# Kernel tuning notes

Measured on AMD Instinct MI355X. Metric: run time of the kernel, lower is better.

The kernel has to match this reference:

```python
import jax, jax.numpy as jnp
import numpy as np

N = 100000          # num nodes
E_C = 6_400_000     # connection edges
E_D = 400_000       # destination edges
F_IN = 5
H = 8
BN_EPS = 1e-5
L2_EPS = 1e-12


def setup_inputs() -> dict:
    key = jax.random.key(0)
    ks = jax.random.split(key, 16)
    d = {}
    d["x"] = jax.random.normal(ks[0], (N, F_IN), dtype=jnp.float32)
    d["edge_index_connections"] = jax.random.randint(ks[1], (2, E_C), 0, N, dtype=jnp.int64)
    d["edge_index_destinations"] = jax.random.randint(ks[2], (2, E_D), 0, N, dtype=jnp.int64)
    # SAGEConv weights: lin_l (neighbor aggregate), lin_r (root), no bias
    d["W1l"] = jax.random.normal(ks[3], (H, F_IN), jnp.float32) * 0.3
    d["W1r"] = jax.random.normal(ks[4], (H, F_IN), jnp.float32) * 0.3
    d["W2l"] = jax.random.normal(ks[5], (H, H), jnp.float32) * 0.3
    d["W2r"] = jax.random.normal(ks[6], (H, H), jnp.float32) * 0.3
    d["W3l"] = jax.random.normal(ks[7], (H, H), jnp.float32) * 0.3
    d["W3r"] = jax.random.normal(ks[8], (H, H), jnp.float32) * 0.3
    d["W4l"] = jax.random.normal(ks[9], (H, H), jnp.float32) * 0.3
    d["W4r"] = jax.random.normal(ks[10], (H, H), jnp.float32) * 0.3
    # LazyBatchNorm1d affine params (init gamma=1, beta=0)
    for i in range(1, 5):
        d[f"g{i}"] = jnp.ones((H,), jnp.float32)
        d[f"b{i}"] = jnp.zeros((H,), jnp.float32)
    return d


def _sage(x, ei, Wl, Wr):
    # PyG SAGEConv(mean aggr, normalize=True, bias=False):
    # out = lin_l(mean_{j in N(i)} x_j) + lin_r(x_i); then L2 normalize rows.
    src, dst = ei[0], ei[1]
    msgs = x[src]                                            # [E, F] gather
    s = jax.ops.segment_sum(msgs, dst, num_segments=N)       # [N, F]
    cnt = jax.ops.segment_sum(jnp.ones((ei.shape[1],), x.dtype), dst, num_segments=N)
    mean = s / jnp.maximum(cnt, 1.0)[:, None]                # zero for isolated nodes
    out = mean @ Wl.T + x @ Wr.T                             # [N, H]
    nrm = jnp.linalg.norm(out, axis=-1, keepdims=True)
    return out / jnp.maximum(nrm, L2_EPS)


def _bn(x, g, b):
    # BatchNorm1d in training mode: per-feature batch stats (biased variance)
    m = x.mean(axis=0)
    v = x.var(axis=0)
    return (x - m) * jax.lax.rsqrt(v + BN_EPS) * g + b


def reference(x, edge_index_connections, edge_index_destinations,
              W1l, W1r, W2l, W2r, W3l, W3r, W4l, W4r,
              g1, b1, g2, b2, g3, b3, g4, b4):
    eic = edge_index_connections
    eid = edge_index_destinations
    h = _bn(jax.nn.relu(_sage(x, eic, W1l, W1r)), g1, b1)
    # ITERATIONS_BEFORE_DESTINATION = 1 (conv4 + bn2)
    h = _bn(jax.nn.relu(_sage(h, eic, W4l, W4r)), g2, b2)
    # destination pass (conv2 + bn3)
    h = _bn(jax.nn.relu(_sage(h, eid, W2l, W2r)), g3, b3)
    # ITERATIONS_AFTER_DESTINATION = 2 (conv3 + bn4)
    for _ in range(2):
        h = _bn(jax.nn.relu(_sage(h, eic, W3l, W3r)), g4, b4)
    return h
```

## Files before the change

kernel.cpp:

```cpp
#include <hip/hip_runtime.h>
#include <hip/hip_fp16.h>

#define NN 100000
#define EC 6400000
#define ED 400000
#define BN_EPS 1e-5f
#define NSB ((NN + 255) >> 8)
#define NCH 256
#define CSR_CAP 19200
#define CHUNK_OF(E) (((((E) + NCH - 1) / NCH) + 3) & ~3)


__global__ __launch_bounds__(1024)
void pre_hist_prep(const int* __restrict__ eic, const int* __restrict__ eid,
                   int* __restrict__ bhist_c, int* __restrict__ bhist_d,
                   const float* __restrict__ x, const float* __restrict__ W1l,
                   const float* __restrict__ W1r, float* __restrict__ xp,
                   __half* __restrict__ xp16,
                   float* __restrict__ W1lp, float* __restrict__ W1rp) {
    int blk = blockIdx.x;
    if (blk < 2 * NCH) {
        const int* ei = (blk < NCH) ? eic : eid;
        int E = (blk < NCH) ? EC : ED;
        int* bhist = (blk < NCH) ? bhist_c : bhist_d;
        int k = (blk < NCH) ? blk : blk - NCH;
        __shared__ int h[NSB];
        for (int i = threadIdx.x; i < NSB; i += 1024) h[i] = 0;
        __syncthreads();
        int chunk = CHUNK_OF(E);
        int beg = k * chunk, end = min(E, beg + chunk);
        for (int e = beg + threadIdx.x * 4; e < end; e += 1024 * 4) {
            int4 d4 = *(const int4*)&ei[E + e];
            atomicAdd(&h[d4.x >> 8], 1);
            atomicAdd(&h[d4.y >> 8], 1);
            atomicAdd(&h[d4.z >> 8], 1);
            atomicAdd(&h[d4.w >> 8], 1);
        }
        __syncthreads();
        for (int i = threadIdx.x; i < NSB; i += 1024) bhist[i * NCH + k] = h[i];
    } else {
        int pb = blk - 2 * NCH;
        int t = pb * 1024 + threadIdx.x;
        if (t < 64) {
            int f = t >> 3, k = t & 7;
            W1lp[t] = (k < 5) ? W1l[f * 5 + k] : 0.f;
            W1rp[t] = (k < 5) ? W1r[f * 5 + k] : 0.f;
        }
        for (int idx = t; idx < NN * 8; idx += 32 * 1024) {
            int f = idx & 7, i = idx >> 3;
            float v = (f < 5) ? x[i * 5 + f] : 0.f;
            xp[idx] = v;
            xp16[idx] = __float2half(v);
        }
    }
}

__global__ __launch_bounds__(256)
void row_scan2(int* __restrict__ bhist_c, int* __restrict__ total_c,
               int* __restrict__ bhist_d, int* __restrict__ total_d) {
    int blk = blockIdx.x;
    int* row = (blk < NSB) ? (bhist_c + blk * NCH)
                           : (bhist_d + (blk - NSB) * NCH);
    int* total = (blk < NSB) ? total_c : total_d;
    int bb = (blk < NSB) ? blk : blk - NSB;
    __shared__ int wsum[4];
    int lane = threadIdx.x & 63, w = threadIdx.x >> 6;
    int v = row[threadIdx.x];
    int x = v;
    #pragma unroll
    for (int sh = 1; sh < 64; sh <<= 1) { int y = __shfl_up(x, sh); if (lane >= sh) x += y; }
    if (lane == 63) wsum[w] = x;
    __syncthreads();
    int wb = 0;
    #pragma unroll
    for (int j = 0; j < 4; ++j) if (j < w) wb += wsum[j];
    row[threadIdx.x] = wb + x - v;
    if (threadIdx.x == 255) total[bb] = wb + x;
}

__global__ void base2(const int* __restrict__ total_c, int* __restrict__ bbase_c,
                      const int* __restrict__ total_d, int* __restrict__ bbase_d,
                      float* __restrict__ stats) {
    for (int i = threadIdx.x; i < 5 * 256; i += 256) stats[i] = 0.f;
    __shared__ int wsum[4];
    __shared__ int carry;
    int lane = threadIdx.x & 63, w = threadIdx.x >> 6;
    for (int which = 0; which < 2; ++which) {
        const int* gt = which ? total_d : total_c;
        int* bb = which ? bbase_d : bbase_c;
        if (threadIdx.x == 0) carry = 0;
        __syncthreads();
        for (int s = 0; s < NSB; s += 256) {
            int idx = s + threadIdx.x;
            int v = (idx < NSB) ? gt[idx] : 0;
            int x = v;
            #pragma unroll
            for (int sh = 1; sh < 64; sh <<= 1) { int y = __shfl_up(x, sh); if (lane >= sh) x += y; }
            if (lane == 63) wsum[w] = x;
            __syncthreads();
            int wb = 0;
            #pragma unroll
            for (int j = 0; j < 4; ++j) if (j < w) wb += wsum[j];
            int all = wsum[0] + wsum[1] + wsum[2] + wsum[3];
            if (idx < NSB) bb[idx] = carry + wb + x - v;
            __syncthreads();
            if (threadIdx.x == 0) carry += all;
            __syncthreads();
        }
    }
}

__global__ __launch_bounds__(1024)
void scatter2(const int* __restrict__ eic, const int* __restrict__ eid,
              const int* __restrict__ bhist_c, const int* __restrict__ bbase_c,
              unsigned* __restrict__ packed_c,
              const int* __restrict__ bhist_d, const int* __restrict__ bbase_d,
              unsigned* __restrict__ packed_d) {
    int blk = blockIdx.x;
    const int* ei = (blk < NCH) ? eic : eid;
    int E = (blk < NCH) ? EC : ED;
    const int* bhist = (blk < NCH) ? bhist_c : bhist_d;
    const int* bbase = (blk < NCH) ? bbase_c : bbase_d;
    unsigned* packed = (blk < NCH) ? packed_c : packed_d;
    int k = (blk < NCH) ? blk : blk - NCH;
    __shared__ int cur[NSB];
    for (int b = threadIdx.x; b < NSB; b += 1024)
        cur[b] = bbase[b] + bhist[b * NCH + k];
    __syncthreads();
    int chunk = CHUNK_OF(E);
    int beg = k * chunk, end = min(E, beg + chunk);
    for (int e = beg + threadIdx.x * 4; e < end; e += 1024 * 4) {
        int4 s4 = *(const int4*)&ei[e];
        int4 d4 = *(const int4*)&ei[E + e];
        { int p = atomicAdd(&cur[d4.x >> 8], 1); packed[p] = (unsigned)s4.x | ((unsigned)(d4.x & 255) << 17); }
        { int p = atomicAdd(&cur[d4.y >> 8], 1); packed[p] = (unsigned)s4.y | ((unsigned)(d4.y & 255) << 17); }
        { int p = atomicAdd(&cur[d4.z >> 8], 1); packed[p] = (unsigned)s4.z | ((unsigned)(d4.z & 255) << 17); }
        { int p = atomicAdd(&cur[d4.w >> 8], 1); packed[p] = (unsigned)s4.w | ((unsigned)(d4.w & 255) << 17); }
    }
}

__global__ __launch_bounds__(256)
void csr2(const unsigned* __restrict__ packed_c, const int* __restrict__ bbase_c,
          const int* __restrict__ total_c, int* __restrict__ csr_c,
          int* __restrict__ offs_c, int* __restrict__ deg_c, float* __restrict__ inv_c,
          const unsigned* __restrict__ packed_d, const int* __restrict__ bbase_d,
          const int* __restrict__ total_d, int* __restrict__ csr_d,
          int* __restrict__ offs_d, int* __restrict__ deg_d, float* __restrict__ inv_d) {
    int blk = blockIdx.x;
    const unsigned* packed = (blk < NSB) ? packed_c : packed_d;
    const int* bbase = (blk < NSB) ? bbase_c : bbase_d;
    const int* total = (blk < NSB) ? total_c : total_d;
    int* csr  = (blk < NSB) ? csr_c : csr_d;
    int* offs = (blk < NSB) ? offs_c : offs_d;
    int* deg  = (blk < NSB) ? deg_c : deg_d;
    float* inv = (blk < NSB) ? inv_c : inv_d;
    int b = (blk < NSB) ? blk : blk - NSB;

    __shared__ int h[256];
    __shared__ int loff[256];
    __shared__ int ws2[4];
    __shared__ int ebuf[CSR_CAP];
    int ebeg = bbase[b], ecnt = total[b];
    int node0 = b << 8;
    int nn = min(256, NN - node0);
    h[threadIdx.x] = 0;
    __syncthreads();
    for (int e = threadIdx.x; e < ecnt; e += 256)
        atomicAdd(&h[packed[ebeg + e] >> 17], 1);
    __syncthreads();
    {
        int lane = threadIdx.x & 63, w = threadIdx.x >> 6;
        int v = h[threadIdx.x], x = v;
        #pragma unroll
        for (int sh = 1; sh < 64; sh <<= 1) { int y = __shfl_up(x, sh); if (lane >= sh) x += y; }
        if (lane == 63) ws2[w] = x;
        __syncthreads();
        int wb = 0;
        #pragma unroll
        for (int j = 0; j < 4; ++j) if (j < w) wb += ws2[j];
        int excl = wb + x - v;
        loff[threadIdx.x] = excl;
        if (threadIdx.x < nn) {
            int node = node0 + threadIdx.x;
            offs[node] = ebeg + excl;
            deg[node]  = v;
            inv[node]  = 1.0f / (float)(v > 1 ? v : 1);
        }
    }
    __syncthreads();
    if (ecnt <= CSR_CAP) {
        for (int e = threadIdx.x; e < ecnt; e += 256) {
            unsigned u = packed[ebeg + e];
            int p = atomicAdd(&loff[u >> 17], 1);
            ebuf[p] = (int)(u & 0x1FFFF);
        }
        __syncthreads();
        for (int e = threadIdx.x; e < ecnt; e += 256) csr[ebeg + e] = ebuf[e];
    } else {
        for (int e = threadIdx.x; e < ecnt; e += 256) {
            unsigned u = packed[ebeg + e];
            int p = atomicAdd(&loff[u >> 17], 1);
            csr[ebeg + p] = (int)(u & 0x1FFFF);
        }
    }
}

template<bool APPLY_BN>
__global__ __launch_bounds__(256)
void sage_layer8(const float* __restrict__ hin,
                 const __half* __restrict__ hin16,
                 const float* __restrict__ stats_in,
                 const float* __restrict__ gin, const float* __restrict__ bin,
                 const int* __restrict__ offs, const int* __restrict__ deg,
                 const int* __restrict__ csr, const float* __restrict__ inv,
                 const float* __restrict__ Wl, const float* __restrict__ Wr,
                 float* __restrict__ hout, __half* __restrict__ hout16,
                 float* __restrict__ stats_out) {
    __shared__ float bl[16];
    int tid = threadIdx.x;
    if (tid < 16) bl[tid] = 0.f;
    __syncthreads();
    int wave = tid >> 6, lane = tid & 63, g = lane >> 3, f = lane & 7;

    float sc[8], sh[8];
    #pragma unroll
    for (int k = 0; k < 8; ++k) { sc[k] = 1.f; sh[k] = 0.f; }
    if constexpr (APPLY_BN) {
        #pragma unroll
        for (int k = 0; k < 8; ++k) {
            float m = stats_in[k * 16] * (1.f / NN);
            float v = stats_in[(8 + k) * 16] * (1.f / NN) - m * m;
            float is = rsqrtf(v + BN_EPS);
            sc[k] = gin[k] * is;
            sh[k] = bin[k] - m * sc[k];
        }
    }
    float wl[8], wr[8];
    #pragma unroll
    for (int k = 0; k < 8; ++k) { wl[k] = Wl[f * 8 + k]; wr[k] = Wr[f * 8 + k]; }

    float acc_r = 0.f, acc_r2 = 0.f;
    const int stride = gridDim.x * 32;
    for (int i0 = (blockIdx.x * 4 + wave) * 8; i0 < NN; i0 += stride) {
        int i = i0 + g;
        int ic = min(i, NN - 1);
        bool ok = (i < NN);
        int d = ok ? deg[ic] : 0;
        int o = offs[ic];
        float a0 = 0, a1 = 0, a2 = 0, a3 = 0, a4 = 0, a5 = 0, a6 = 0, a7 = 0;
        for (int b = 0; b < d; b += 8) {
            int e = b + f;
            int cv = csr[o + e];
            float m = (e < d) ? 1.f : 0.f;
            unsigned s = min((unsigned)cv & 0x1FFFFu, (unsigned)(NN - 1));
            uint4 rv = *(const uint4*)(hin16 + (size_t)s * 8);
            float2 p0 = __half22float2(*(const __half2*)&rv.x);
            float2 p1 = __half22float2(*(const __half2*)&rv.y);
            float2 p2 = __half22float2(*(const __half2*)&rv.z);
            float2 p3 = __half22float2(*(const __half2*)&rv.w);
            a0 = fmaf(p0.x, m, a0); a1 = fmaf(p0.y, m, a1);
            a2 = fmaf(p1.x, m, a2); a3 = fmaf(p1.y, m, a3);
            a4 = fmaf(p2.x, m, a4); a5 = fmaf(p2.y, m, a5);
            a6 = fmaf(p3.x, m, a6); a7 = fmaf(p3.y, m, a7);
        }
        #pragma unroll
        for (int msk = 1; msk < 8; msk <<= 1) {
            a0 += __shfl_xor(a0, msk); a1 += __shfl_xor(a1, msk);
            a2 += __shfl_xor(a2, msk); a3 += __shfl_xor(a3, msk);
            a4 += __shfl_xor(a4, msk); a5 += __shfl_xor(a5, msk);
            a6 += __shfl_xor(a6, msk); a7 += __shfl_xor(a7, msk);
        }
        float im = inv[ic];
        float dnz = (d > 0) ? 1.f : 0.f;
        const float4* hp = (const float4*)(hin + (size_t)ic * 8);
        float4 h0 = hp[0];
        float4 h1 = hp[1];
        float hk[8] = { h0.x, h0.y, h0.z, h0.w, h1.x, h1.y, h1.z, h1.w };
        float ac[8] = { a0, a1, a2, a3, a4, a5, a6, a7 };
        float y = 0.f;
        #pragma unroll
        for (int k = 0; k < 8; ++k) {
            float mk = fmaf(sc[k], ac[k] * im, sh[k] * dnz);
            float hh = fmaf(sc[k], hk[k], sh[k]);
            y = fmaf(mk, wl[k], y);
            y = fmaf(hh, wr[k], y);
        }
        float n2 = y * y;
        n2 += __shfl_xor(n2, 1);
        n2 += __shfl_xor(n2, 2);
        n2 += __shfl_xor(n2, 4);
        float z = y / fmaxf(sqrtf(n2), 1e-12f);
        float r = fmaxf(z, 0.f);
        r = ok ? r : 0.f;
        if (ok) {
            hout[(size_t)i * 8 + f] = r;
            hout16[(size_t)i * 8 + f] = __float2half(r);
        }
        acc_r += r;
        acc_r2 += r * r;
    }
    atomicAdd(&bl[f], acc_r);
    atomicAdd(&bl[8 + f], acc_r2);
    __syncthreads();
    if (tid < 16) atomicAdd(&stats_out[tid * 16], bl[tid]);
}

__global__ void apply_bn_out(const float* __restrict__ hin,
                             const float* __restrict__ stats,
                             const float* __restrict__ g, const float* __restrict__ b,
                             float* __restrict__ out) {
    int t = blockIdx.x * blockDim.x + threadIdx.x;
    if (t >= NN * 8) return;
    int f = t & 7;
    float m = stats[f * 16] * (1.0f / NN);
    float v = stats[(8 + f) * 16] * (1.0f / NN) - m * m;
    float sc = g[f] * rsqrtf(v + BN_EPS);
    float sh = b[f] - m * sc;
    out[t] = fmaf(hin[t], sc, sh);
}


static inline char* bump(char*& p, size_t bytes) {
    char* r = p;
    p += (bytes + 255) & ~(size_t)255;
    return r;
}

extern "C" void kernel_launch(void* const* d_in, const int* in_sizes, int n_in,
                              void* d_out, int out_size, void* d_ws, size_t ws_size,
                              hipStream_t stream) {
    const float* x   = (const float*)d_in[0];
    const int* eic   = (const int*)d_in[1];
    const int* eid   = (const int*)d_in[2];
    const float* W1l = (const float*)d_in[3];
    const float* W1r = (const float*)d_in[4];
    const float* W2l = (const float*)d_in[5];
    const float* W2r = (const float*)d_in[6];
    const float* W3l = (const float*)d_in[7];
    const float* W3r = (const float*)d_in[8];
    const float* W4l = (const float*)d_in[9];
    const float* W4r = (const float*)d_in[10];
    const float* g1 = (const float*)d_in[11];
    const float* b1 = (const float*)d_in[12];
    const float* g2 = (const float*)d_in[13];
    const float* b2 = (const float*)d_in[14];
    const float* g3 = (const float*)d_in[15];
    const float* b3 = (const float*)d_in[16];
    const float* g4 = (const float*)d_in[17];
    const float* b4 = (const float*)d_in[18];
    float* out = (float*)d_out;

    char* p = (char*)d_ws;
    float* stats   = (float*)bump(p, 5 * 256 * 4);
    int*   bhist_c = (int*)  bump(p, (size_t)NSB * NCH * 4);
    int*   bhist_d = (int*)  bump(p, (size_t)NSB * NCH * 4);
    int*   total_c = (int*)  bump(p, NSB * 4);
    int*   bbase_c = (int*)  bump(p, NSB * 4);
    int*   total_d = (int*)  bump(p, NSB * 4);
    int*   bbase_d = (int*)  bump(p, NSB * 4);
    int*   offs_c  = (int*)  bump(p, NN * 4);
    int*   deg_c   = (int*)  bump(p, NN * 4);
    float* inv_c   = (float*)bump(p, NN * 4);
    int*   offs_d  = (int*)  bump(p, NN * 4);
    int*   deg_d   = (int*)  bump(p, NN * 4);
    float* inv_d   = (float*)bump(p, NN * 4);
    int*   csr_c   = (int*)  bump(p, ((size_t)EC + 64) * 4);
    int*   csr_d   = (int*)  bump(p, ((size_t)ED + 64) * 4);
    float* xp32    = (float*)bump(p, (size_t)NN * 8 * 4);
    __half* xp16   = (__half*)bump(p, (size_t)NN * 8 * 2);
    float* W1lp    = (float*)bump(p, 64 * 4);
    float* W1rp    = (float*)bump(p, 64 * 4);
    unsigned* packed_d = (unsigned*)bump(p, (size_t)ED * 4);
    char* pc = p;
    unsigned* packed_c = (unsigned*)bump(p, (size_t)EC * 4);
    char* pr = pc;
    float*  r_a   = (float*) bump(pr, (size_t)NN * 8 * 4);
    float*  r_b   = (float*) bump(pr, (size_t)NN * 8 * 4);
    __half* h16_a = (__half*)bump(pr, (size_t)NN * 8 * 2);
    __half* h16_b = (__half*)bump(pr, (size_t)NN * 8 * 2);
    (void)ws_size; (void)in_sizes; (void)n_in; (void)out_size;

    pre_hist_prep<<<2 * NCH + 32, 1024, 0, stream>>>(
        eic, eid, bhist_c, bhist_d, x, W1l, W1r, xp32, xp16, W1lp, W1rp);
    row_scan2<<<2 * NSB, 256, 0, stream>>>(bhist_c, total_c, bhist_d, total_d);
    base2<<<1, 256, 0, stream>>>(total_c, bbase_c, total_d, bbase_d, stats);
    scatter2<<<2 * NCH, 1024, 0, stream>>>(
        eic, eid, bhist_c, bbase_c, packed_c, bhist_d, bbase_d, packed_d);
    csr2<<<2 * NSB, 256, 0, stream>>>(
        packed_c, bbase_c, total_c, csr_c, offs_c, deg_c, inv_c,
        packed_d, bbase_d, total_d, csr_d, offs_d, deg_d, inv_d);

    const int LB = 2048;
    sage_layer8<false><<<LB, 256, 0, stream>>>(
        xp32, xp16, nullptr, nullptr, nullptr,
        offs_c, deg_c, csr_c, inv_c, W1lp, W1rp, r_a, h16_a, stats + 0);
    sage_layer8<true><<<LB, 256, 0, stream>>>(
        r_a, h16_a, stats + 0, g1, b1,
        offs_c, deg_c, csr_c, inv_c, W4l, W4r, r_b, h16_b, stats + 256);
    sage_layer8<true><<<LB, 256, 0, stream>>>(
        r_b, h16_b, stats + 256, g2, b2,
        offs_d, deg_d, csr_d, inv_d, W2l, W2r, r_a, h16_a, stats + 512);
    sage_layer8<true><<<LB, 256, 0, stream>>>(
        r_a, h16_a, stats + 512, g3, b3,
        offs_c, deg_c, csr_c, inv_c, W3l, W3r, r_b, h16_b, stats + 768);
    sage_layer8<true><<<LB, 256, 0, stream>>>(
        r_b, h16_b, stats + 768, g4, b4,
        offs_c, deg_c, csr_c, inv_c, W3l, W3r, r_a, h16_a, stats + 1024);
    apply_bn_out<<<(NN * 8 + 255) / 256, 256, 0, stream>>>(r_a, stats + 1024, g4, b4, out);
}
```

Baseline: 615.8 us.

## Unroll neighbor gather to four edges per lane and fold BN into weights

Each lane now handles four consecutive CSR entries per iteration (32 edges per group step instead of 8), so four independent 16-byte row gathers are in flight per lane. This raises memory-level parallelism for degree-64 nodes. The batch-norm scale and shift are folded into the layer weights plus a constant bias, which shortens the per-node epilogue, and the root-row and inverse-degree loads are hoisted ahead of the gather loop. The trade-offs are more registers per lane and reads of the CSR slot past the degree; those extra gathers are masked to row 0 and could touch memory beyond the array end.

Result: faster. 580.6 us (-5.7%).

```diff
diff --git a/kernel.cpp b/kernel.cpp
--- a/kernel.cpp
+++ b/kernel.cpp
@@ -205,6 +205,17 @@
     }
 }
 
+#define ACC8(RV, M) do { \
+    float2 q0 = __half22float2(*(const __half2*)&RV.x); \
+    float2 q1 = __half22float2(*(const __half2*)&RV.y); \
+    float2 q2 = __half22float2(*(const __half2*)&RV.z); \
+    float2 q3 = __half22float2(*(const __half2*)&RV.w); \
+    a0 = fmaf(q0.x, M, a0); a1 = fmaf(q0.y, M, a1); \
+    a2 = fmaf(q1.x, M, a2); a3 = fmaf(q1.y, M, a3); \
+    a4 = fmaf(q2.x, M, a4); a5 = fmaf(q2.y, M, a5); \
+    a6 = fmaf(q3.x, M, a6); a7 = fmaf(q3.y, M, a7); \
+} while (0)
+
 template<bool APPLY_BN>
 __global__ __launch_bounds__(256)
 void sage_layer8(const float* __restrict__ hin,
@@ -222,22 +233,24 @@
     __syncthreads();
     int wave = tid >> 6, lane = tid & 63, g = lane >> 3, f = lane & 7;
 
-    float sc[8], sh[8];
+    float wls[8], wrs[8];
+    float Bl = 0.f, Br = 0.f;
     #pragma unroll
-    for (int k = 0; k < 8; ++k) { sc[k] = 1.f; sh[k] = 0.f; }
-    if constexpr (APPLY_BN) {
-        #pragma unroll
-        for (int k = 0; k < 8; ++k) {
+    for (int k = 0; k < 8; ++k) {
+        float w_l = Wl[f * 8 + k], w_r = Wr[f * 8 + k];
+        float sck = 1.f, shk = 0.f;
+        if constexpr (APPLY_BN) {
             float m = stats_in[k * 16] * (1.f / NN);
             float v = stats_in[(8 + k) * 16] * (1.f / NN) - m * m;
             float is = rsqrtf(v + BN_EPS);
-            sc[k] = gin[k] * is;
-            sh[k] = bin[k] - m * sc[k];
-        }
-    }
-    float wl[8], wr[8];
-    #pragma unroll
-    for (int k = 0; k < 8; ++k) { wl[k] = Wl[f * 8 + k]; wr[k] = Wr[f * 8 + k]; }
+            sck = gin[k] * is;
+            shk = bin[k] - m * sck;
+        }
+        wls[k] = sck * w_l;
+        wrs[k] = sck * w_r;
+        Bl = fmaf(shk, w_l, Bl);
+        Br = fmaf(shk, w_r, Br);
+    }
 
     float acc_r = 0.f, acc_r2 = 0.f;
     const int stride = gridDim.x * 32;
@@ -247,21 +260,32 @@
         bool ok = (i < NN);
         int d = ok ? deg[ic] : 0;
         int o = offs[ic];
+        float im = inv[ic];
+        const float4* hp = (const float4*)(hin + (size_t)ic * 8);
+        float4 h0 = hp[0];
+        float4 h1 = hp[1];
         float a0 = 0, a1 = 0, a2 = 0, a3 = 0, a4 = 0, a5 = 0, a6 = 0, a7 = 0;
-        for (int b = 0; b < d; b += 8) {
-            int e = b + f;
-            int cv = csr[o + e];
-            float m = (e < d) ? 1.f : 0.f;
-            unsigned s = min((unsigned)cv & 0x1FFFFu, (unsigned)(NN - 1));
-            uint4 rv = *(const uint4*)(hin16 + (size_t)s * 8);
-            float2 p0 = __half22float2(*(const __half2*)&rv.x);
-            float2 p1 = __half22float2(*(const __half2*)&rv.y);
-            float2 p2 = __half22float2(*(const __half2*)&rv.z);
-            float2 p3 = __half22float2(*(const __half2*)&rv.w);
-            a0 = fmaf(p0.x, m, a0); a1 = fmaf(p0.y, m, a1);
-            a2 = fmaf(p1.x, m, a2); a3 = fmaf(p1.y, m, a3);
-            a4 = fmaf(p2.x, m, a4); a5 = fmaf(p2.y, m, a5);
-            a6 = fmaf(p3.x, m, a6); a7 = fmaf(p3.y, m, a7);
+        for (int b = 0; b < d; b += 32) {
+            int e = b + f * 4;
+            const int* cp = csr + o + e;
+            int c0 = cp[0], c1 = cp[1], c2 = cp[2], c3 = cp[3];
+            bool k0 = (e < d), k1 = (e + 1 < d), k2 = (e + 2 < d), k3 = (e + 3 < d);
+            unsigned s0 = k0 ? ((unsigned)c0 & 0x1FFFFu) : 0u;
+            unsigned s1 = k1 ? ((unsigned)c1 & 0x1FFFFu) : 0u;
+            unsigned s2 = k2 ? ((unsigned)c2 & 0x1FFFFu) : 0u;
+            unsigned s3 = k3 ? ((unsigned)c3 & 0x1FFFFu) : 0u;
+            uint4 r0 = *(const uint4*)(hin16 + (size_t)s0 * 8);
+            uint4 r1 = *(const uint4*)(hin16 + (size_t)s1 * 8);
+            uint4 r2 = *(const uint4*)(hin16 + (size_t)s2 * 8);
+            uint4 r3 = *(const uint4*)(hin16 + (size_t)s3 * 8);
+            float m0 = k0 ? 1.f : 0.f;
+            float m1 = k1 ? 1.f : 0.f;
+            float m2 = k2 ? 1.f : 0.f;
+            float m3 = k3 ? 1.f : 0.f;
+            ACC8(r0, m0);
+            ACC8(r1, m1);
+            ACC8(r2, m2);
+            ACC8(r3, m3);
         }
         #pragma unroll
         for (int msk = 1; msk < 8; msk <<= 1) {
@@ -270,20 +294,14 @@
             a4 += __shfl_xor(a4, msk); a5 += __shfl_xor(a5, msk);
             a6 += __shfl_xor(a6, msk); a7 += __shfl_xor(a7, msk);
         }
-        float im = inv[ic];
         float dnz = (d > 0) ? 1.f : 0.f;
-        const float4* hp = (const float4*)(hin + (size_t)ic * 8);
-        float4 h0 = hp[0];
-        float4 h1 = hp[1];
         float hk[8] = { h0.x, h0.y, h0.z, h0.w, h1.x, h1.y, h1.z, h1.w };
         float ac[8] = { a0, a1, a2, a3, a4, a5, a6, a7 };
-        float y = 0.f;
+        float y = fmaf(dnz, Bl, Br);
         #pragma unroll
         for (int k = 0; k < 8; ++k) {
-            float mk = fmaf(sc[k], ac[k] * im, sh[k] * dnz);
-            float hh = fmaf(sc[k], hk[k], sh[k]);
-            y = fmaf(mk, wl[k], y);
-            y = fmaf(hh, wr[k], y);
+            y = fmaf(ac[k] * im, wls[k], y);
+            y = fmaf(hk[k], wrs[k], y);
         }
         float n2 = y * y;
         n2 += __shfl_xor(n2, 1);
```
